# Kernel tuning notes

Hardware: AMD Instinct MI355X
Metric: run time of the kernel (lower is better)

## Reference

```python
import jax, jax.numpy as jnp
import numpy as np

N = 100000      # nodes
E = 1200000     # edges (avg degree ~12)
D_IN = 64
D_OUT = 64


def setup_inputs() -> dict:
    key = jax.random.key(0)
    k1, k2, k3, k4 = jax.random.split(key, 4)
    x = jax.random.normal(k1, (N, D_IN), dtype=jnp.float32)
    # learned params (glorot-ish init)
    W = jax.random.normal(k2, (D_IN, D_OUT), dtype=jnp.float32) / np.sqrt(D_IN).astype(np.float32)
    b = jnp.zeros((D_OUT,), dtype=jnp.float32)
    src = jax.random.randint(k3, (E,), 0, N, dtype=jnp.int32)
    dst = jax.random.randint(k4, (E,), 0, N, dtype=jnp.int32)
    return {"x": x, "W": W, "b": b, "src": src, "dst": dst}


def reference(x, W, b, src, dst):
    # GCN layer: h = relu( D^-1/2 A D^-1/2 (x @ W) + b ), dropout=0 (eval)
    ones = jnp.ones(src.shape[0], dtype=x.dtype)
    deg_out = jax.ops.segment_sum(ones, src, num_segments=N)   # out-degree of source nodes
    deg_in = jax.ops.segment_sum(ones, dst, num_segments=N)    # in-degree of dest nodes
    norm_src = jax.lax.rsqrt(jnp.maximum(deg_out, 1.0))
    norm_dst = jax.lax.rsqrt(jnp.maximum(deg_in, 1.0))

    h = x @ W                                                  # [N, D_OUT] dense transform
    msg = h[src] * norm_src[src][:, None]                      # [E, D_OUT] gathered, pre-normalized messages
    agg = jax.ops.segment_sum(msg, dst, num_segments=N)        # [N, D_OUT] sparse aggregation
    out = agg * norm_dst[:, None] + b
    return jax.nn.relu(out)
```

## Files before the change

### kernel.cpp

```cpp
#include <hip/hip_runtime.h>
#include <hip/hip_bf16.h>

#define N_NODES 100000
#define N_EDGES 1200000
#define DCH 64

#define HB 96
#define CHUNK ((N_EDGES + HB - 1) / HB)
#define HALF_BINS 50000
#define HALF_WORDS 12500

#define BNODES 256
#define KBUK ((N_NODES + BNODES - 1) / BNODES)
#define CAPE 6144

#define HISTB (2 * HB)
#define GEMMB 384

#define OFF_DEG      0
#define OFF_GCUR     100096
#define OFF_FLAG     101760
#define OFF_ESORT    102144
#define OFF_HS       9711616

__device__ __forceinline__ float load_f(const void* p, int i, int f32) {
    if (f32) return ((const float*)p)[i];
    return __bfloat162float(((const __hip_bfloat16*)p)[i]);
}

__device__ __forceinline__ unsigned short f2bf_bits(float f) {
    __hip_bfloat16 h = __float2bfloat16(f);
    return __builtin_bit_cast(unsigned short, h);
}

__global__ __launch_bounds__(1024)
void fused_kernel(const int* __restrict__ src,
                  const int* __restrict__ dst,
                  const void* __restrict__ x,
                  const void* __restrict__ W,
                  unsigned int* __restrict__ deg_packed,
                  int* __restrict__ gcur,
                  unsigned int* __restrict__ esort,
                  int* __restrict__ flag,
                  __hip_bfloat16* __restrict__ hs) {
    __shared__ unsigned int h[HALF_WORDS];
    int tid = threadIdx.x;
    int bid = blockIdx.x;

    if (bid < HB) {
        int* cnt  = (int*)h;
        int* base = cnt + KBUK;
        int* cur  = base + KBUK;
        for (int i = tid; i < KBUK; i += 1024) { cnt[i] = 0; cur[i] = 0; }
        __syncthreads();
        int e0 = bid * CHUNK;
        const int2* src2 = (const int2*)(src + e0);
        const int2* dst2 = (const int2*)(dst + e0);
        int npair = CHUNK >> 1;
        for (int p = tid; p < npair; p += 1024) {
            int2 dp = dst2[p];
            atomicAdd(&cnt[dp.x >> 8], 1);
            atomicAdd(&cnt[dp.y >> 8], 1);
        }
        __syncthreads();
        for (int i = tid; i < KBUK; i += 1024)
            base[i] = atomicAdd(&gcur[i], cnt[i]);
        __syncthreads();
        for (int p = tid; p < npair; p += 1024) {
            int2 sp = src2[p];
            int2 dp = dst2[p];
            int b0 = dp.x >> 8, b1 = dp.y >> 8;
            int pos0 = base[b0] + atomicAdd(&cur[b0], 1);
            if (pos0 < CAPE)
                esort[b0 * CAPE + pos0] =
                    (unsigned int)sp.x | ((unsigned int)(dp.x & 255) << 24);
            int pos1 = base[b1] + atomicAdd(&cur[b1], 1);
            if (pos1 < CAPE)
                esort[b1 * CAPE + pos1] =
                    (unsigned int)sp.y | ((unsigned int)(dp.y & 255) << 24);
        }
        if (bid == 0) {
            __syncthreads();
            if (tid == 0) cnt[0] = 0;
            __syncthreads();
            if (tid < 256) {
                const unsigned short* u = (const unsigned short*)x;
                int c = 0;
                for (int i = tid * 16; i < tid * 16 + 16; ++i) {
                    unsigned short v = u[2 * i];
                    int e = (v >> 7) & 0xFF;
                    if (e >= 141) c++;
                }
                if (c) atomicAdd(&cnt[0], c);
            }
            __syncthreads();
            if (tid == 0) *flag = (cnt[0] > 256) ? 1 : 0;
        }
    } else if (bid < HB + HISTB) {
        int hb = bid - HB;
        int b = hb >> 1, half = hb & 1;
        for (int w = tid; w < HALF_WORDS; w += 1024) h[w] = 0;
        __syncthreads();
        int lo = half * HALF_BINS;
        int e0 = b * CHUNK;
        const int2* src2 = (const int2*)(src + e0);
        int npair = CHUNK >> 1;
        for (int p = tid; p < npair; p += 1024) {
            int2 sp = src2[p];
            int n0 = sp.x - lo, n1 = sp.y - lo;
            if ((unsigned)n0 < (unsigned)HALF_BINS)
                atomicAdd(&h[n0 >> 2], 1u << ((n0 & 3) * 8));
            if ((unsigned)n1 < (unsigned)HALF_BINS)
                atomicAdd(&h[n1 >> 2], 1u << ((n1 & 3) * 8));
        }
        __syncthreads();
        unsigned int* dp = deg_packed + half * HALF_WORDS;
        for (int w = tid; w < HALF_WORDS; w += 1024) {
            unsigned int v = h[w];
            if (v) atomicAdd(&dp[w], v);
        }
    } else {
        int* sn = (int*)h;
        if (tid == 0) sn[0] = 0;
        __syncthreads();
        if (tid < 256) {
            const unsigned short* u = (const unsigned short*)x;
            int c = 0;
            for (int i = tid * 16; i < tid * 16 + 16; ++i) {
                unsigned short v = u[2 * i];
                int e = (v >> 7) & 0xFF;
                if (e >= 141) c++;
            }
            if (c) atomicAdd(sn, c);
        }
        __syncthreads();
        int f32 = sn[0] > 256;

        int lane = tid & 63;
        int wave = ((bid - (HB + HISTB)) * 1024 + tid) >> 6;
        const int nwaves = (GEMMB * 1024) >> 6;
        float wcol[DCH];
#pragma unroll
        for (int k = 0; k < DCH; ++k)
            wcol[k] = load_f(W, k * DCH + lane, f32);
        for (int node = wave; node < N_NODES; node += nwaves) {
            float xv = load_f(x, node * DCH + lane, f32);
            float s0 = 0.0f, s1 = 0.0f, s2 = 0.0f, s3 = 0.0f;
#pragma unroll
            for (int k = 0; k < DCH; k += 4) {
                float x0 = __int_as_float(__builtin_amdgcn_readlane(__float_as_int(xv), k + 0));
                float x1 = __int_as_float(__builtin_amdgcn_readlane(__float_as_int(xv), k + 1));
                float x2 = __int_as_float(__builtin_amdgcn_readlane(__float_as_int(xv), k + 2));
                float x3 = __int_as_float(__builtin_amdgcn_readlane(__float_as_int(xv), k + 3));
                s0 = fmaf(x0, wcol[k + 0], s0);
                s1 = fmaf(x1, wcol[k + 1], s1);
                s2 = fmaf(x2, wcol[k + 2], s2);
                s3 = fmaf(x3, wcol[k + 3], s3);
            }
            float sum = (s0 + s1) + (s2 + s3);
            hs[node * DCH + lane] = __float2bfloat16(sum);
        }
    }
}

__global__ __launch_bounds__(1024)
void sortgather_kernel(const __hip_bfloat16* __restrict__ hs,
                       const unsigned int* __restrict__ esort,
                       const int* __restrict__ gcur,
                       const unsigned int* __restrict__ deg_packed,
                       const void* __restrict__ b,
                       const int* __restrict__ flag,
                       void* __restrict__ out) {
    __shared__ unsigned int ebuf[CAPE];
    __shared__ int cnt[BNODES];
    __shared__ int loc[BNODES];
    __shared__ int sc[BNODES];
    __shared__ int cur[BNODES];
    __shared__ float tab[256];
    int k = blockIdx.x, tid = threadIdx.x;
    int bbase = k * CAPE;
    int m = gcur[k];
    if (m > CAPE) m = CAPE;

    if (tid < BNODES) { cnt[tid] = 0; cur[tid] = 0; }
    if (tid < 256) tab[tid] = rsqrtf(fmaxf((float)tid, 1.0f));
    __syncthreads();
    for (int e = tid; e < m; e += 1024)
        atomicAdd(&cnt[esort[bbase + e] >> 24], 1);
    __syncthreads();
    int v = 0;
    if (tid < BNODES) { v = cnt[tid]; sc[tid] = v; }
    __syncthreads();
    for (int off = 1; off < BNODES; off <<= 1) {
        int add = 0;
        if (tid < BNODES && tid >= off) add = sc[tid - off];
        __syncthreads();
        if (tid < BNODES) sc[tid] += add;
        __syncthreads();
    }
    if (tid < BNODES) loc[tid] = sc[tid] - v;
    __syncthreads();
    for (int e = tid; e < m; e += 1024) {
        unsigned int w = esort[bbase + e];
        int r = w >> 24;
        unsigned int s = w & 0xFFFFFFu;
        unsigned int dw = deg_packed[s >> 2];
        unsigned int degb = (dw >> ((s & 3) * 8)) & 0xFFu;
        int pos = loc[r] + atomicAdd(&cur[r], 1);
        ebuf[pos] = s | (degb << 24);
    }
    __syncthreads();

    int f32 = *flag;
    int lane = tid & 63, wv = tid >> 6;
    int q = lane >> 4;
    int cg = lane & 15;
    const unsigned short* hsu = (const unsigned short*)hs;
    float b0 = load_f(b, cg * 4 + 0, f32);
    float b1 = load_f(b, cg * 4 + 1, f32);
    float b2 = load_f(b, cg * 4 + 2, f32);
    float b3 = load_f(b, cg * 4 + 3, f32);
    int nlo = k * BNODES;
    for (int base = wv; base < BNODES; base += 32) {
        int tA = base, tB = base + 16;
        int nodeA = nlo + tA, nodeB = nlo + tB;
        int begA = loc[tA], degA = cnt[tA];
        int begB = loc[tB], degB = cnt[tB];
        float4 aA0 = {0.f,0.f,0.f,0.f}, aA1 = {0.f,0.f,0.f,0.f};
        float4 aB0 = {0.f,0.f,0.f,0.f}, aB1 = {0.f,0.f,0.f,0.f};
        int dmax = degA > degB ? degA : degB;
        for (int j0 = 0; j0 < dmax; j0 += 8) {
            int i0 = j0 + q, i1 = j0 + 4 + q;
            unsigned int wA0 = ebuf[(i0 < degA) ? (begA + i0) : 0];
            unsigned int wA1 = ebuf[(i1 < degA) ? (begA + i1) : 0];
            unsigned int wB0 = ebuf[(i0 < degB) ? (begB + i0) : 0];
            unsigned int wB1 = ebuf[(i1 < degB) ? (begB + i1) : 0];
            unsigned int sA0 = wA0 & 0xFFFFFFu, sA1 = wA1 & 0xFFFFFFu;
            unsigned int sB0 = wB0 & 0xFFFFFFu, sB1 = wB1 & 0xFFFFFFu;
            float fA0 = tab[wA0 >> 24], fA1 = tab[wA1 >> 24];
            float fB0 = tab[wB0 >> 24], fB1 = tab[wB1 >> 24];
            uint2 uA0 = ((const uint2*)(hsu + sA0 * DCH))[cg];
            uint2 uA1 = ((const uint2*)(hsu + sA1 * DCH))[cg];
            uint2 uB0 = ((const uint2*)(hsu + sB0 * DCH))[cg];
            uint2 uB1 = ((const uint2*)(hsu + sB1 * DCH))[cg];
            if (i0 < degA) {
                aA0.x = fmaf(__uint_as_float(uA0.x << 16),        fA0, aA0.x);
                aA0.y = fmaf(__uint_as_float(uA0.x & 0xFFFF0000u), fA0, aA0.y);
                aA0.z = fmaf(__uint_as_float(uA0.y << 16),        fA0, aA0.z);
                aA0.w = fmaf(__uint_as_float(uA0.y & 0xFFFF0000u), fA0, aA0.w);
            }
            if (i1 < degA) {
                aA1.x = fmaf(__uint_as_float(uA1.x << 16),        fA1, aA1.x);
                aA1.y = fmaf(__uint_as_float(uA1.x & 0xFFFF0000u), fA1, aA1.y);
                aA1.z = fmaf(__uint_as_float(uA1.y << 16),        fA1, aA1.z);
                aA1.w = fmaf(__uint_as_float(uA1.y & 0xFFFF0000u), fA1, aA1.w);
            }
            if (i0 < degB) {
                aB0.x = fmaf(__uint_as_float(uB0.x << 16),        fB0, aB0.x);
                aB0.y = fmaf(__uint_as_float(uB0.x & 0xFFFF0000u), fB0, aB0.y);
                aB0.z = fmaf(__uint_as_float(uB0.y << 16),        fB0, aB0.z);
                aB0.w = fmaf(__uint_as_float(uB0.y & 0xFFFF0000u), fB0, aB0.w);
            }
            if (i1 < degB) {
                aB1.x = fmaf(__uint_as_float(uB1.x << 16),        fB1, aB1.x);
                aB1.y = fmaf(__uint_as_float(uB1.x & 0xFFFF0000u), fB1, aB1.y);
                aB1.z = fmaf(__uint_as_float(uB1.y << 16),        fB1, aB1.z);
                aB1.w = fmaf(__uint_as_float(uB1.y & 0xFFFF0000u), fB1, aB1.w);
            }
        }
        float4 oA, oB;
        oA.x = aA0.x + aA1.x; oA.y = aA0.y + aA1.y;
        oA.z = aA0.z + aA1.z; oA.w = aA0.w + aA1.w;
        oB.x = aB0.x + aB1.x; oB.y = aB0.y + aB1.y;
        oB.z = aB0.z + aB1.z; oB.w = aB0.w + aB1.w;
        oA.x += __shfl_xor(oA.x, 16); oA.y += __shfl_xor(oA.y, 16);
        oA.z += __shfl_xor(oA.z, 16); oA.w += __shfl_xor(oA.w, 16);
        oA.x += __shfl_xor(oA.x, 32); oA.y += __shfl_xor(oA.y, 32);
        oA.z += __shfl_xor(oA.z, 32); oA.w += __shfl_xor(oA.w, 32);
        oB.x += __shfl_xor(oB.x, 16); oB.y += __shfl_xor(oB.y, 16);
        oB.z += __shfl_xor(oB.z, 16); oB.w += __shfl_xor(oB.w, 16);
        oB.x += __shfl_xor(oB.x, 32); oB.y += __shfl_xor(oB.y, 32);
        oB.z += __shfl_xor(oB.z, 32); oB.w += __shfl_xor(oB.w, 32);
        int myNode = (lane < 16) ? nodeA : nodeB;
        int myDeg  = (lane < 16) ? degA : degB;
        float4 o   = (lane < 16) ? oA : oB;
        if (lane < 32 && myNode < N_NODES) {
            float nrm = rsqrtf(fmaxf((float)myDeg, 1.0f));
            o.x = fmaxf(o.x * nrm + b0, 0.0f);
            o.y = fmaxf(o.y * nrm + b1, 0.0f);
            o.z = fmaxf(o.z * nrm + b2, 0.0f);
            o.w = fmaxf(o.w * nrm + b3, 0.0f);
            if (f32) {
                ((float4*)out)[myNode * 16 + cg] = o;
            } else {
                ushort4 s;
                s.x = f2bf_bits(o.x);
                s.y = f2bf_bits(o.y);
                s.z = f2bf_bits(o.z);
                s.w = f2bf_bits(o.w);
                ((ushort4*)out)[myNode * 16 + cg] = s;
            }
        }
    }
}

extern "C" void kernel_launch(void* const* d_in, const int* in_sizes, int n_in,
                              void* d_out, int out_size, void* d_ws, size_t ws_size,
                              hipStream_t stream) {
    const void* x   = d_in[0];
    const void* W   = d_in[1];
    const void* b   = d_in[2];
    const int*  src = (const int*)d_in[3];
    const int*  dst = (const int*)d_in[4];

    char* ws = (char*)d_ws;
    unsigned int* deg_packed = (unsigned int*)(ws + OFF_DEG);
    int* gcur     = (int*)(ws + OFF_GCUR);
    int* flag     = (int*)(ws + OFF_FLAG);
    unsigned int* esort = (unsigned int*)(ws + OFF_ESORT);
    __hip_bfloat16* hs  = (__hip_bfloat16*)(ws + OFF_HS);

    (void)hipMemsetAsync(ws, 0, OFF_FLAG + 4, stream);

    fused_kernel<<<HB + HISTB + GEMMB, 1024, 0, stream>>>(
        src, dst, x, W, deg_packed, gcur, esort, flag, hs);

    sortgather_kernel<<<KBUK, 1024, 0, stream>>>(
        hs, esort, gcur, deg_packed, b, flag, d_out);
}
```

Baseline: 166.7 us.

## Halve fused kernel block size, double sort blocks, two-node GEMM via LDS weights

Shrinks the fused kernel's block size from 1024 to 512 threads and sets a launch bound of 6 blocks per CU. The edge-sorting stage now uses twice as many blocks, each covering a smaller edge chunk. The dense transform stages W transposed in shared memory with padding and reads it as float4 rows. Each wave then computes two nodes per iteration, sharing those weights and giving more independent FMA chains. The aim is better occupancy and latency hiding, at the cost of more global atomics on the bucket cursors and extra block launches.

```diff
diff --git a/kernel.cpp b/kernel.cpp
--- a/kernel.cpp
+++ b/kernel.cpp
@@ -5,17 +5,23 @@
 #define N_EDGES 1200000
 #define DCH 64
 
+#define NT 512
+
+#define SB 192
+#define SCHUNK (N_EDGES / SB)
+
 #define HB 96
-#define CHUNK ((N_EDGES + HB - 1) / HB)
+#define CHUNK (N_EDGES / HB)
 #define HALF_BINS 50000
 #define HALF_WORDS 12500
+
+#define GEMMB 384
+#define GWAVES (GEMMB * NT / 64)
+
 
 #define BNODES 256
 #define KBUK ((N_NODES + BNODES - 1) / BNODES)
 #define CAPE 6144
-
-#define HISTB (2 * HB)
-#define GEMMB 384
 
 #define OFF_DEG      0
 #define OFF_GCUR     100096
@@ -33,7 +39,7 @@
     return __builtin_bit_cast(unsigned short, h);
 }
 
-__global__ __launch_bounds__(1024)
+__global__ __launch_bounds__(NT, 6)
 void fused_kernel(const int* __restrict__ src,
                   const int* __restrict__ dst,
                   const void* __restrict__ x,
@@ -47,26 +53,26 @@
     int tid = threadIdx.x;
     int bid = blockIdx.x;
 
-    if (bid < HB) {
+    if (bid < SB) {
         int* cnt  = (int*)h;
         int* base = cnt + KBUK;
         int* cur  = base + KBUK;
-        for (int i = tid; i < KBUK; i += 1024) { cnt[i] = 0; cur[i] = 0; }
-        __syncthreads();
-        int e0 = bid * CHUNK;
+        for (int i = tid; i < KBUK; i += NT) { cnt[i] = 0; cur[i] = 0; }
+        __syncthreads();
+        int e0 = bid * SCHUNK;
         const int2* src2 = (const int2*)(src + e0);
         const int2* dst2 = (const int2*)(dst + e0);
-        int npair = CHUNK >> 1;
-        for (int p = tid; p < npair; p += 1024) {
+        int npair = SCHUNK >> 1;
+        for (int p = tid; p < npair; p += NT) {
             int2 dp = dst2[p];
             atomicAdd(&cnt[dp.x >> 8], 1);
             atomicAdd(&cnt[dp.y >> 8], 1);
         }
         __syncthreads();
-        for (int i = tid; i < KBUK; i += 1024)
+        for (int i = tid; i < KBUK; i += NT)
             base[i] = atomicAdd(&gcur[i], cnt[i]);
         __syncthreads();
-        for (int p = tid; p < npair; p += 1024) {
+        for (int p = tid; p < npair; p += NT) {
             int2 sp = src2[p];
             int2 dp = dst2[p];
             int b0 = dp.x >> 8, b1 = dp.y >> 8;
@@ -96,16 +102,16 @@
             __syncthreads();
             if (tid == 0) *flag = (cnt[0] > 256) ? 1 : 0;
         }
-    } else if (bid < HB + HISTB) {
-        int hb = bid - HB;
-        int b = hb >> 1, half = hb & 1;
-        for (int w = tid; w < HALF_WORDS; w += 1024) h[w] = 0;
+    } else if (bid < SB + 2 * HB) {
+        int hb = bid - SB;
+        int c = hb >> 1, half = hb & 1;
+        for (int w = tid; w < HALF_WORDS; w += NT) h[w] = 0;
         __syncthreads();
         int lo = half * HALF_BINS;
-        int e0 = b * CHUNK;
+        int e0 = c * CHUNK;
         const int2* src2 = (const int2*)(src + e0);
         int npair = CHUNK >> 1;
-        for (int p = tid; p < npair; p += 1024) {
+        for (int p = tid; p < npair; p += NT) {
             int2 sp = src2[p];
             int n0 = sp.x - lo, n1 = sp.y - lo;
             if ((unsigned)n0 < (unsigned)HALF_BINS)
@@ -115,7 +121,7 @@
         }
         __syncthreads();
         unsigned int* dp = deg_packed + half * HALF_WORDS;
-        for (int w = tid; w < HALF_WORDS; w += 1024) {
+        for (int w = tid; w < HALF_WORDS; w += NT) {
             unsigned int v = h[w];
             if (v) atomicAdd(&dp[w], v);
         }
@@ -135,31 +141,51 @@
         }
         __syncthreads();
         int f32 = sn[0] > 256;
+        __syncthreads();
+
+        float* wt = (float*)h;
+        for (int i = tid; i < DCH * DCH; i += NT) {
+            int kk = i >> 6, cc = i & 63;
+            wt[cc * 68 + kk] = load_f(W, i, f32);
+        }
+        __syncthreads();
 
         int lane = tid & 63;
-        int wave = ((bid - (HB + HISTB)) * 1024 + tid) >> 6;
-        const int nwaves = (GEMMB * 1024) >> 6;
-        float wcol[DCH];
-#pragma unroll
-        for (int k = 0; k < DCH; ++k)
-            wcol[k] = load_f(W, k * DCH + lane, f32);
-        for (int node = wave; node < N_NODES; node += nwaves) {
-            float xv = load_f(x, node * DCH + lane, f32);
-            float s0 = 0.0f, s1 = 0.0f, s2 = 0.0f, s3 = 0.0f;
-#pragma unroll
-            for (int k = 0; k < DCH; k += 4) {
-                float x0 = __int_as_float(__builtin_amdgcn_readlane(__float_as_int(xv), k + 0));
-                float x1 = __int_as_float(__builtin_amdgcn_readlane(__float_as_int(xv), k + 1));
-                float x2 = __int_as_float(__builtin_amdgcn_readlane(__float_as_int(xv), k + 2));
-                float x3 = __int_as_float(__builtin_amdgcn_readlane(__float_as_int(xv), k + 3));
-                s0 = fmaf(x0, wcol[k + 0], s0);
-                s1 = fmaf(x1, wcol[k + 1], s1);
-                s2 = fmaf(x2, wcol[k + 2], s2);
-                s3 = fmaf(x3, wcol[k + 3], s3);
-            }
-            float sum = (s0 + s1) + (s2 + s3);
-            hs[node * DCH + lane] = __float2bfloat16(sum);
-        }
+        const float4* wrow = (const float4*)(wt + lane * 68);
+        float4 wq0 = wrow[0],  wq1 = wrow[1],  wq2 = wrow[2],  wq3 = wrow[3];
+        float4 wq4 = wrow[4],  wq5 = wrow[5],  wq6 = wrow[6],  wq7 = wrow[7];
+        float4 wq8 = wrow[8],  wq9 = wrow[9],  wq10 = wrow[10], wq11 = wrow[11];
+        float4 wq12 = wrow[12], wq13 = wrow[13], wq14 = wrow[14], wq15 = wrow[15];
+
+        int wave = ((bid - (SB + 2 * HB)) * NT + tid) >> 6;
+#define RLA(i) __int_as_float(__builtin_amdgcn_readlane(xiA, (i)))
+#define RLB(i) __int_as_float(__builtin_amdgcn_readlane(xiB, (i)))
+#define GRP(j, V) \
+    a0 = fmaf(RLA(4*(j)+0), (V).x, a0); a1 = fmaf(RLA(4*(j)+1), (V).y, a1); \
+    a2 = fmaf(RLA(4*(j)+2), (V).z, a2); a3 = fmaf(RLA(4*(j)+3), (V).w, a3); \
+    c0 = fmaf(RLB(4*(j)+0), (V).x, c0); c1 = fmaf(RLB(4*(j)+1), (V).y, c1); \
+    c2 = fmaf(RLB(4*(j)+2), (V).z, c2); c3 = fmaf(RLB(4*(j)+3), (V).w, c3);
+
+        for (int node = wave; node < N_NODES; node += 2 * GWAVES) {
+            int nodeB = node + GWAVES;
+            int hasB = nodeB < N_NODES;
+            float xvA = load_f(x, node * DCH + lane, f32);
+            float xvB = hasB ? load_f(x, nodeB * DCH + lane, f32) : 0.0f;
+            int xiA = __float_as_int(xvA);
+            int xiB = __float_as_int(xvB);
+            float a0 = 0.f, a1 = 0.f, a2 = 0.f, a3 = 0.f;
+            float c0 = 0.f, c1 = 0.f, c2 = 0.f, c3 = 0.f;
+            GRP(0, wq0)   GRP(1, wq1)   GRP(2, wq2)   GRP(3, wq3)
+            GRP(4, wq4)   GRP(5, wq5)   GRP(6, wq6)   GRP(7, wq7)
+            GRP(8, wq8)   GRP(9, wq9)   GRP(10, wq10) GRP(11, wq11)
+            GRP(12, wq12) GRP(13, wq13) GRP(14, wq14) GRP(15, wq15)
+            hs[node * DCH + lane] = __float2bfloat16((a0 + a1) + (a2 + a3));
+            if (hasB)
+                hs[nodeB * DCH + lane] = __float2bfloat16((c0 + c1) + (c2 + c3));
+        }
+#undef RLA
+#undef RLB
+#undef GRP
     }
 }
 
@@ -322,7 +348,7 @@
 
     (void)hipMemsetAsync(ws, 0, OFF_FLAG + 4, stream);
 
-    fused_kernel<<<HB + HISTB + GEMMB, 1024, 0, stream>>>(
+    fused_kernel<<<SB + 2 * HB + GEMMB, NT, 0, stream>>>(
         src, dst, x, W, deg_packed, gcur, esort, flag, hs);
 
     sortgather_kernel<<<KBUK, 1024, 0, stream>>>(
```

Measured after the change: 183.9 us. 10.3% more time.
